# Kernel tuning notes

Hardware: AMD Instinct MI355X
Metric: run time of the kernel (lower is better)

The kernel has to match this reference:

```python
import jax, jax.numpy as jnp
import numpy as np

WS = 8      # window size
HEADS = 8

def setup_inputs() -> dict:
    key = jax.random.key(0)
    ks = jax.random.split(key, 8)
    b, dim, H, W = 128, 224, 32, 32
    inner = 224  # dim_head(28) * heads(8)
    n_win = (H // WS) * (W // WS)  # 16, matches seq_l2
    return {
        "x": jax.random.normal(ks[0], (b, dim, H, W), dtype=jnp.float32),
        "Wq": jax.random.normal(ks[1], (dim, inner), dtype=jnp.float32) * 0.02,
        "Wk": jax.random.normal(ks[2], (dim, inner), dtype=jnp.float32) * 0.02,
        "Wv": jax.random.normal(ks[3], (dim, inner), dtype=jnp.float32) * 0.02,
        "Wo": jax.random.normal(ks[4], (inner, dim), dtype=jnp.float32) * 0.02,
        "bo": jax.random.normal(ks[5], (dim,), dtype=jnp.float32) * 0.02,
        "pos_emb": jax.random.normal(ks[6], (1, 1, HEADS, n_win, n_win), dtype=jnp.float32),
        "scale": jnp.ones((1,), dtype=jnp.float32),
    }

def _forward(x, Wq, Wk, Wv, Wo, bo, pos_emb, scale):
    b, c, H, W = x.shape
    nh, nw = H // WS, W // WS
    n = nh * nw            # number of windows (attention length)
    m = WS * WS            # positions inside a window
    inner = Wq.shape[1]
    d = inner // HEADS

    xh = x.transpose(0, 2, 3, 1)                       # [b,H,W,c]
    q = xh @ Wq
    k = xh @ Wk
    v = xh @ Wv                                        # [b,H,W,inner]

    def win(t):
        # b (nh ws) (nw ws) c -> b m h n d  (attend across windows per in-window pos)
        t = t.reshape(b, nh, WS, nw, WS, inner)
        t = t.transpose(0, 1, 3, 2, 4, 5).reshape(b, n, m, inner)
        t = t.transpose(0, 2, 1, 3)                    # [b,m,n,inner]
        t = t.reshape(b, m, n, HEADS, d).transpose(0, 1, 3, 2, 4)
        return t                                       # [b,m,h,n,d]

    q2, k2, v2 = win(q), win(k), win(v)
    q2 = q2 * scale
    sim = jnp.einsum('bmhid,bmhjd->bmhij', q2, k2) + pos_emb  # [b,m,h,n,n]
    attn = jax.nn.softmax(sim, axis=-1)
    o = jnp.einsum('bmhij,bmhjd->bmhid', attn, v2)     # [b,m,h,n,d]

    o = o.transpose(0, 1, 3, 2, 4).reshape(b, m, n, inner)  # b m n (h d)
    o = o.transpose(0, 2, 1, 3)                        # [b,n,m,inner]
    o = o @ Wo + bo                                    # [b,n,m,c]
    o = o.reshape(b, nh, nw, WS, WS, c).transpose(0, 1, 3, 2, 4, 5)
    o = o.reshape(b, H, W, c)
    return o.transpose(0, 3, 1, 2)                     # [b,c,H,W]

def reference(x, Wq, Wk, Wv, Wo, bo, pos_emb, scale):
    return _forward(x, Wq, Wk, Wv, Wo, bo, pos_emb, scale)
```

## Files before the change

kernel.cpp:

```cpp
#include <hip/hip_runtime.h>
#include <stdint.h>

#define NB   128
#define CC   224
#define NWIN 16
#define DH   28
#define NHEADS 8

using bf16x8 = __attribute__((ext_vector_type(8))) short;
using u16x4  = __attribute__((ext_vector_type(4))) unsigned short;
using f32x4  = __attribute__((ext_vector_type(4))) float;

__device__ inline unsigned short f2bf(float f) {
    union { float f; unsigned u; } v; v.f = f;
    unsigned u = v.u;
    u += 0x7fffu + ((u >> 16) & 1u);
    return (unsigned short)(u >> 16);
}

__global__ void prep_weights(const float* __restrict__ Wq, const float* __restrict__ Wk,
                             const float* __restrict__ Wv, const float* __restrict__ Wo,
                             unsigned short* __restrict__ wt) {
    int e = blockIdx.x * blockDim.x + threadIdx.x;
    if (e >= 4 * CC * CC) return;
    int c   = e >> 9;
    int r   = e & 511;
    int l   = r >> 3, j = r & 7;
    int kk  = c % 7;
    int t   = c / 7;
    int sel = t / 14, ntl = t % 14;
    int n = ntl * 16 + (l & 15);
    int k = kk * 32 + (l >> 4) * 8 + j;
    const float* W = (sel == 0) ? Wq : (sel == 1) ? Wk : (sel == 2) ? Wv : Wo;
    wt[e] = f2bf(W[k * CC + n]);
}

#define QS_OFF   0
#define XS_OFF   14848
#define KS_OFF   32768
#define ATT_OFF  47616
#define SMEM_BYTES 52736

__global__ void __launch_bounds__(512, 6) attn_fused(
    const float* __restrict__ x, const unsigned short* __restrict__ wt,
    const float* __restrict__ bo, const float* __restrict__ pos,
    const float* __restrict__ scale, float* __restrict__ out)
{
    extern __shared__ char smem[];
    unsigned short* qs   = (unsigned short*)(smem + QS_OFF);
    unsigned short* xs   = (unsigned short*)(smem + XS_OFF);
    unsigned short* ks   = (unsigned short*)(smem + KS_OFF);
    unsigned short* att  = (unsigned short*)(smem + ATT_OFF);
    unsigned short* vt   = xs;
    unsigned short* ob   = qs;
    float*          oout = (float*)(smem + XS_OFF);

    const int tid = threadIdx.x;
    const int wv  = tid >> 6;
    const int l   = tid & 63;
    const int g   = l >> 4;
    const int li  = l & 15;

    const int bid = blockIdx.x;
    const int xcd = bid & 7;
    const int idx = bid >> 3;
    const int hq  = idx & 3;
    const int wg  = (xcd << 7) + (idx >> 2);
    const int bi  = wg >> 3;
    const int mr  = wg & 7;

    {
        const float* xb = x + ((size_t)bi * CC << 10);
        for (int q = tid; q < CC * NWIN; q += 512) {
            int ch = q >> 4, wx = q & 15;
            int wi = wx >> 2, wj = wx & 3;
            int h = wi * 8 + mr, w0 = wj * 8 + hq * 2;
            float2 v2 = *(const float2*)(xb + (ch << 10) + (h << 5) + w0);
            xs[wx * 232 + ch]        = f2bf(v2.x);
            xs[(wx + 16) * 232 + ch] = f2bf(v2.y);
        }
    }
    const float scl = scale[0];
    __syncthreads();

    const int mt = wv & 1;
    const int arow = mt * 16 + li;
    bf16x8 a1f[7];
    #pragma unroll
    for (int kk = 0; kk < 7; ++kk)
        a1f[kk] = *(const bf16x8*)(xs + arow * 232 + kk * 32 + g * 8);
    __syncthreads();

    for (int ntg = wv >> 1; ntg < 42; ntg += 4) {
        int sel = ntg / 14, ntl = ntg % 14;
        const unsigned short* wsel = wt + (size_t)ntg * 3584 + l * 8;
        f32x4 acc = {0.f, 0.f, 0.f, 0.f};
        #pragma unroll
        for (int kk = 0; kk < 7; ++kk) {
            bf16x8 bf = *(const bf16x8*)(wsel + kk * 512);
            acc = __builtin_amdgcn_mfma_f32_16x16x32_bf16(a1f[kk], bf, acc, 0, 0, 0);
        }
        int colb = ntl * 16 + li;
        #pragma unroll
        for (int r = 0; r < 4; ++r) {
            int row = mt * 16 + g * 4 + r;
            float v = acc[r];
            if (sel == 0)      qs[row * 232 + colb] = f2bf(v * scl);
            else if (sel == 1) ks[row * 232 + colb] = f2bf(v);
            else               vt[colb * 40 + row]  = f2bf(v);
        }
    }
    __syncthreads();

    const int hd = wv;
    const int cb = hd * DH;
    float pv4[4];
    #pragma unroll
    for (int r = 0; r < 4; ++r)
        pv4[r] = pos[(hd * 16 + g * 4 + r) * 16 + li];
    f32x4 sim[2];
    #pragma unroll
    for (int mc2 = 0; mc2 < 2; ++mc2) {
        int rowq = li + mc2 * 16;
        bf16x8 aq, bk;
        const unsigned short* qp = qs + rowq * 232 + cb + g * 8;
        const unsigned short* kp = ks + rowq * 232 + cb + g * 8;
        u16x4 qlo = *(const u16x4*)qp, qhi = *(const u16x4*)(qp + 4);
        u16x4 klo = *(const u16x4*)kp, khi = *(const u16x4*)(kp + 4);
        if (g == 3) { qhi = (u16x4)0; khi = (u16x4)0; }
        #pragma unroll
        for (int j = 0; j < 4; ++j) {
            aq[j] = (short)qlo[j]; aq[4 + j] = (short)qhi[j];
            bk[j] = (short)klo[j]; bk[4 + j] = (short)khi[j];
        }
        f32x4 z = {0.f, 0.f, 0.f, 0.f};
        sim[mc2] = __builtin_amdgcn_mfma_f32_16x16x32_bf16(aq, bk, z, 0, 0, 0);
    }
    __syncthreads();

    {
        unsigned short* attw = att + wv * (16 * 20);
        for (int mc2 = 0; mc2 < 2; ++mc2) {
            #pragma unroll
            for (int r = 0; r < 4; ++r) {
                int i = g * 4 + r;
                float s = sim[mc2][r] + pv4[r];
                float mx = s;
                mx = fmaxf(mx, __shfl_xor(mx, 1, 16));
                mx = fmaxf(mx, __shfl_xor(mx, 2, 16));
                mx = fmaxf(mx, __shfl_xor(mx, 4, 16));
                mx = fmaxf(mx, __shfl_xor(mx, 8, 16));
                float e = __expf(s - mx);
                float sm = e;
                sm += __shfl_xor(sm, 1, 16);
                sm += __shfl_xor(sm, 2, 16);
                sm += __shfl_xor(sm, 4, 16);
                sm += __shfl_xor(sm, 8, 16);
                attw[i * 20 + li] = f2bf(e / sm);
            }
            bf16x8 pa;
            if (g < 2) {
                const unsigned short* ap = attw + li * 20 + g * 8;
                u16x4 alo = *(const u16x4*)ap, ahi = *(const u16x4*)(ap + 4);
                #pragma unroll
                for (int j = 0; j < 4; ++j) { pa[j] = (short)alo[j]; pa[4 + j] = (short)ahi[j]; }
            } else {
                pa = (bf16x8)0;
            }
            for (int dt = 0; dt < 2; ++dt) {
                bf16x8 bv;
                if (g < 2) {
                    bv = *(const bf16x8*)(vt + (cb + dt * 16 + li) * 40 + mc2 * 16 + g * 8);
                } else {
                    bv = (bf16x8)0;
                }
                f32x4 po = {0.f, 0.f, 0.f, 0.f};
                po = __builtin_amdgcn_mfma_f32_16x16x32_bf16(pa, bv, po, 0, 0, 0);
                int dh = dt * 16 + li;
                if (dh < DH) {
                    #pragma unroll
                    for (int r = 0; r < 4; ++r) {
                        int i = g * 4 + r;
                        ob[(i + mc2 * 16) * 232 + cb + dh] = f2bf(po[r]);
                    }
                }
            }
        }
    }
    __syncthreads();

    bf16x8 a3f[7];
    #pragma unroll
    for (int kk = 0; kk < 7; ++kk)
        a3f[kk] = *(const bf16x8*)(ob + arow * 232 + kk * 32 + g * 8);
    __syncthreads();

    for (int ntl = wv >> 1; ntl < 14; ntl += 4) {
        const unsigned short* wsel = wt + (size_t)(42 + ntl) * 3584 + l * 8;
        f32x4 acc = {0.f, 0.f, 0.f, 0.f};
        #pragma unroll
        for (int kk = 0; kk < 7; ++kk) {
            bf16x8 bf = *(const bf16x8*)(wsel + kk * 512);
            acc = __builtin_amdgcn_mfma_f32_16x16x32_bf16(a3f[kk], bf, acc, 0, 0, 0);
        }
        int colb = ntl * 16 + li;
        #pragma unroll
        for (int r = 0; r < 4; ++r) {
            int row = mt * 16 + g * 4 + r;
            oout[row * 225 + colb] = acc[r];
        }
    }
    __syncthreads();

    {
        float* outb = out + ((size_t)bi * CC << 10);
        for (int q = tid; q < CC * NWIN; q += 512) {
            int ch = q >> 4, wx = q & 15;
            int wi = wx >> 2, wj = wx & 3;
            int h = wi * 8 + mr, w0 = wj * 8 + hq * 2;
            float b = bo[ch];
            float2 v2;
            v2.x = oout[wx * 225 + ch] + b;
            v2.y = oout[(wx + 16) * 225 + ch] + b;
            *(float2*)(outb + (ch << 10) + (h << 5) + w0) = v2;
        }
    }
}

extern "C" void kernel_launch(void* const* d_in, const int* in_sizes, int n_in,
                              void* d_out, int out_size, void* d_ws, size_t ws_size,
                              hipStream_t stream) {
    const float* x   = (const float*)d_in[0];
    const float* Wq  = (const float*)d_in[1];
    const float* Wk  = (const float*)d_in[2];
    const float* Wv  = (const float*)d_in[3];
    const float* Wo  = (const float*)d_in[4];
    const float* bo  = (const float*)d_in[5];
    const float* pos = (const float*)d_in[6];
    const float* scl = (const float*)d_in[7];
    float* out = (float*)d_out;
    unsigned short* wt = (unsigned short*)d_ws;

    prep_weights<<<dim3((4 * CC * CC + 255) / 256), dim3(256), 0, stream>>>(Wq, Wk, Wv, Wo, wt);

    (void)hipFuncSetAttribute((const void*)attn_fused,
                              hipFuncAttributeMaxDynamicSharedMemorySize, SMEM_BYTES);
    attn_fused<<<dim3(NB * 8 * 4), dim3(512), SMEM_BYTES, stream>>>(x, wt, bo, pos, scl, out);
}
```

Before: 153.4 us.

## Have each wave compute both row tiles to reuse weight fragments across MFMAs

Each wave now keeps A fragments for both 16-row M tiles in registers. For every weight B fragment it loads from global memory, it issues two MFMAs. Work is split over 8 waves by column tile, where before it was split over 4 wave pairs, so each weight fragment is fetched once per workgroup instead of twice. The extra A fragments and accumulators raise register use, so the launch bound drops from 6 to 4 blocks per CU, which may lower occupancy.

```diff
diff --git a/kernel.cpp b/kernel.cpp
--- a/kernel.cpp
+++ b/kernel.cpp
@@ -41,7 +41,7 @@
 #define ATT_OFF  47616
 #define SMEM_BYTES 52736
 
-__global__ void __launch_bounds__(512, 6) attn_fused(
+__global__ void __launch_bounds__(512, 4) attn_fused(
     const float* __restrict__ x, const unsigned short* __restrict__ wt,
     const float* __restrict__ bo, const float* __restrict__ pos,
     const float* __restrict__ scale, float* __restrict__ out)
@@ -83,31 +83,39 @@
     const float scl = scale[0];
     __syncthreads();
 
-    const int mt = wv & 1;
-    const int arow = mt * 16 + li;
-    bf16x8 a1f[7];
-    #pragma unroll
-    for (int kk = 0; kk < 7; ++kk)
-        a1f[kk] = *(const bf16x8*)(xs + arow * 232 + kk * 32 + g * 8);
-    __syncthreads();
-
-    for (int ntg = wv >> 1; ntg < 42; ntg += 4) {
+    bf16x8 a0f[7], a1f[7];
+    #pragma unroll
+    for (int kk = 0; kk < 7; ++kk) {
+        a0f[kk] = *(const bf16x8*)(xs + li * 232 + kk * 32 + g * 8);
+        a1f[kk] = *(const bf16x8*)(xs + (16 + li) * 232 + kk * 32 + g * 8);
+    }
+    __syncthreads();
+
+    for (int ntg = wv; ntg < 42; ntg += 8) {
         int sel = ntg / 14, ntl = ntg % 14;
         const unsigned short* wsel = wt + (size_t)ntg * 3584 + l * 8;
-        f32x4 acc = {0.f, 0.f, 0.f, 0.f};
+        f32x4 acc0 = {0.f, 0.f, 0.f, 0.f}, acc1 = {0.f, 0.f, 0.f, 0.f};
         #pragma unroll
         for (int kk = 0; kk < 7; ++kk) {
             bf16x8 bf = *(const bf16x8*)(wsel + kk * 512);
-            acc = __builtin_amdgcn_mfma_f32_16x16x32_bf16(a1f[kk], bf, acc, 0, 0, 0);
+            acc0 = __builtin_amdgcn_mfma_f32_16x16x32_bf16(a0f[kk], bf, acc0, 0, 0, 0);
+            acc1 = __builtin_amdgcn_mfma_f32_16x16x32_bf16(a1f[kk], bf, acc1, 0, 0, 0);
         }
         int colb = ntl * 16 + li;
         #pragma unroll
         for (int r = 0; r < 4; ++r) {
-            int row = mt * 16 + g * 4 + r;
-            float v = acc[r];
-            if (sel == 0)      qs[row * 232 + colb] = f2bf(v * scl);
-            else if (sel == 1) ks[row * 232 + colb] = f2bf(v);
-            else               vt[colb * 40 + row]  = f2bf(v);
+            int row0 = g * 4 + r, row1 = row0 + 16;
+            float v0 = acc0[r], v1 = acc1[r];
+            if (sel == 0) {
+                qs[row0 * 232 + colb] = f2bf(v0 * scl);
+                qs[row1 * 232 + colb] = f2bf(v1 * scl);
+            } else if (sel == 1) {
+                ks[row0 * 232 + colb] = f2bf(v0);
+                ks[row1 * 232 + colb] = f2bf(v1);
+            } else {
+                vt[colb * 40 + row0] = f2bf(v0);
+                vt[colb * 40 + row1] = f2bf(v1);
+            }
         }
     }
     __syncthreads();
@@ -189,25 +197,29 @@
     }
     __syncthreads();
 
-    bf16x8 a3f[7];
-    #pragma unroll
-    for (int kk = 0; kk < 7; ++kk)
-        a3f[kk] = *(const bf16x8*)(ob + arow * 232 + kk * 32 + g * 8);
-    __syncthreads();
-
-    for (int ntl = wv >> 1; ntl < 14; ntl += 4) {
+    bf16x8 b0f[7], b1f[7];
+    #pragma unroll
+    for (int kk = 0; kk < 7; ++kk) {
+        b0f[kk] = *(const bf16x8*)(ob + li * 232 + kk * 32 + g * 8);
+        b1f[kk] = *(const bf16x8*)(ob + (16 + li) * 232 + kk * 32 + g * 8);
+    }
+    __syncthreads();
+
+    for (int ntl = wv; ntl < 14; ntl += 8) {
         const unsigned short* wsel = wt + (size_t)(42 + ntl) * 3584 + l * 8;
-        f32x4 acc = {0.f, 0.f, 0.f, 0.f};
+        f32x4 acc0 = {0.f, 0.f, 0.f, 0.f}, acc1 = {0.f, 0.f, 0.f, 0.f};
         #pragma unroll
         for (int kk = 0; kk < 7; ++kk) {
             bf16x8 bf = *(const bf16x8*)(wsel + kk * 512);
-            acc = __builtin_amdgcn_mfma_f32_16x16x32_bf16(a3f[kk], bf, acc, 0, 0, 0);
+            acc0 = __builtin_amdgcn_mfma_f32_16x16x32_bf16(b0f[kk], bf, acc0, 0, 0, 0);
+            acc1 = __builtin_amdgcn_mfma_f32_16x16x32_bf16(b1f[kk], bf, acc1, 0, 0, 0);
         }
         int colb = ntl * 16 + li;
         #pragma unroll
         for (int r = 0; r < 4; ++r) {
-            int row = mt * 16 + g * 4 + r;
-            oout[row * 225 + colb] = acc[r];
+            int row0 = g * 4 + r;
+            oout[row0 * 225 + colb]        = acc0[r];
+            oout[(row0 + 16) * 225 + colb] = acc1[r];
         }
     }
     __syncthreads();
```

Measured after the change: 162.8 us. 6.1% more time.
